# Kernel optimization log

Hardware: AMD Instinct MI355X
Metric: run time of the kernel (lower is better)

Reference implementation:

```python
import jax, jax.numpy as jnp
import numpy as np
from jax import lax

BZ, CAPACITY, SEQ_LEN, IN_VAR, N_EDGES = 64, 134, 288, 16, 96


def setup_inputs() -> dict:
    key = jax.random.key(0)
    ks = jax.random.split(key, 9)
    s_gcn = 1.0 / np.sqrt(SEQ_LEN)
    s_conv = 1.0 / np.sqrt(IN_VAR * 3)
    s_fc = 1.0 / np.sqrt(2 * IN_VAR)
    return {
        "src": jax.random.normal(ks[0], (BZ, CAPACITY, SEQ_LEN, IN_VAR), dtype=jnp.float32),
        "feature_edge_index": jax.random.randint(ks[1], (2, N_EDGES), 0, IN_VAR, dtype=jnp.int32),
        # SAGEConv(seq_len, seq_len): out = lin_l(mean_neighbors) + lin_r(x); lin_l has bias
        "Wl": jax.random.uniform(ks[2], (SEQ_LEN, SEQ_LEN), jnp.float32, -s_gcn, s_gcn),
        "Wr": jax.random.uniform(ks[3], (SEQ_LEN, SEQ_LEN), jnp.float32, -s_gcn, s_gcn),
        "b_gcn": jax.random.uniform(ks[4], (SEQ_LEN,), jnp.float32, -s_gcn, s_gcn),
        "conv1_w": jax.random.uniform(ks[5], (IN_VAR, IN_VAR, 3), jnp.float32, -s_conv, s_conv),
        "conv2_w": jax.random.uniform(ks[6], (IN_VAR, IN_VAR, 5), jnp.float32, -s_conv, s_conv),
        "fc_w": jax.random.uniform(ks[7], (IN_VAR, 2 * IN_VAR), jnp.float32, -s_fc, s_fc),
        "fc_b": jax.random.uniform(ks[8], (IN_VAR,), jnp.float32, -s_fc, s_fc),
    }


def reference(src, feature_edge_index, Wl, Wr, b_gcn, conv1_w, conv2_w, fc_w, fc_b):
    bz, cap, S, F = src.shape  # [bz, capacity, seq_len, in_var]
    B = bz * cap
    # node features for the feature graph: [B, in_var, seq_len]
    x2 = src.transpose(0, 1, 3, 2).reshape(B, F, S)
    e_src, e_dst = feature_edge_index[0], feature_edge_index[1]
    # SAGEConv mean aggregation over shared edge_index, vectorized across B graphs
    gathered = x2[:, e_src, :]                                   # [B, E, S]
    agg = jnp.zeros_like(x2).at[:, e_dst, :].add(gathered)       # [B, F, S]
    deg = jnp.zeros((F,), x2.dtype).at[e_dst].add(1.0)
    mean = agg / jnp.maximum(deg, 1.0)[None, :, None]
    feat = (jnp.einsum('bns,ts->bnt', mean, Wl)
            + jnp.einsum('bns,ts->bnt', x2, Wr) + b_gcn)          # [B, F, S]
    fea_fea = feat.reshape(bz, cap, F, S).transpose(0, 1, 3, 2)   # [bz,cap,S,F]
    # dual temporal Conv1d branches (same padding, no bias) on [B, F, S]
    dn = ('NCH', 'OIH', 'NCH')
    c1 = lax.conv_general_dilated(x2, conv1_w, (1,), [(1, 1)], dimension_numbers=dn)
    c2 = lax.conv_general_dilated(x2, conv2_w, (2,), [(2, 2)][:1] * 1, dimension_numbers=dn) if False else lax.conv_general_dilated(x2, conv2_w, (1,), [(2, 2)], dimension_numbers=dn)
    temporal = (c1 + c2).transpose(0, 2, 1).reshape(bz, cap, S, F)
    com = jnp.concatenate([fea_fea, temporal], axis=-1)           # [bz,cap,S,2F]
    com = jnp.einsum('bcsf,of->bcso', com, fc_w) + fc_b
    # dropout is identity in eval mode
    return src + com
```

## Files before the change

### kernel.cpp

```cpp
#include <hip/hip_runtime.h>
#include <hip/hip_bf16.h>

typedef short short8 __attribute__((ext_vector_type(8)));
typedef float float4v __attribute__((ext_vector_type(4)));
typedef unsigned short ushort4v __attribute__((ext_vector_type(4)));

#define BTOT 8576
#define SEQ 288
#define NF 16
#define NB 4
#define SPN 296
#define XTROWS 294
#define XT_USH (XTROWS * 16)
#define XN_USH (16 * SPN)
#define PBN (XT_USH + XN_USH)
#define WCVW 104

__device__ __forceinline__ unsigned short f2b(float f) {
    union { float f; unsigned u; } v; v.f = f;
    unsigned r = v.u + 0x7FFF + ((v.u >> 16) & 1);
    return (unsigned short)(r >> 16);
}
__device__ __forceinline__ float b2f(unsigned short u) {
    union { unsigned u; float f; } v; v.u = ((unsigned)u) << 16; return v.f;
}

__global__ void wcast_kernel(const float* __restrict__ a, const float* __restrict__ b,
                             unsigned short* __restrict__ o) {
    int i = blockIdx.x * 256 + threadIdx.x;
    o[i]         = f2b(a[i]);
    o[82944 + i] = f2b(b[i]);
}

template<int WPRE>
__device__ __forceinline__ short8 ldw(const unsigned short* __restrict__ wb,
                                      const float* __restrict__ wf, int idx) {
    if (WPRE) {
        return *(const short8*)&wb[idx];
    } else {
        const float* p = &wf[idx];
        float4 w0 = *(const float4*)p, w1 = *(const float4*)(p + 4);
        short8 a;
        a[0] = (short)f2b(w0.x); a[1] = (short)f2b(w0.y);
        a[2] = (short)f2b(w0.z); a[3] = (short)f2b(w0.w);
        a[4] = (short)f2b(w1.x); a[5] = (short)f2b(w1.y);
        a[6] = (short)f2b(w1.z); a[7] = (short)f2b(w1.w);
        return a;
    }
}

#define LDB(KK9, B_) do {                                                      \
    const int s0_ = (KK9) * 32;                                                \
    (B_)[0] = *(const short8*)&xsN0[li * SPN + s0_ + 8 * g];                   \
    (B_)[1] = *(const short8*)&xsN1[li * SPN + s0_ + 8 * g];                   \
    (B_)[2] = *(const short8*)&xsN2[li * SPN + s0_ + 8 * g];                   \
    (B_)[3] = *(const short8*)&xsN3[li * SPN + s0_ + 8 * g];                   \
} while (0)

#define LDA(WT_, WF_, KK9, A_) do {                                            \
    const int s0_ = (KK9) * 32;                                                \
    _Pragma("unroll")                                                          \
    for (int m_ = 0; m_ < 3; ++m_)                                             \
        if (m_ < nt) (A_)[m_] = ldw<WPRE>(WT_, WF_, arow[m_] + s0_ + 8 * g);   \
} while (0)

#define MFK(A_, B_) do {                                                       \
    _Pragma("unroll")                                                          \
    for (int m_ = 0; m_ < 3; ++m_)                                             \
        if (m_ < nt) {                                                         \
            _Pragma("unroll")                                                  \
            for (int n_ = 0; n_ < NB; ++n_)                                    \
                acc[m_][n_] = __builtin_amdgcn_mfma_f32_16x16x32_bf16((A_)[m_], (B_)[n_], acc[m_][n_], 0, 0, 0); \
        }                                                                      \
} while (0)

#define GEMM9(WT_, WF_) do {                                                   \
    short8 aC[3], aN[3];                                                       \
    LDA(WT_, WF_, 0, aC);                                                      \
    LDA(WT_, WF_, 1, aN);                                                      \
    _Pragma("unroll")                                                          \
    for (int kk = 0; kk < 9; ++kk) {                                           \
        short8 bb[NB];                                                         \
        LDB(kk, bb);                                                           \
        if (kk & 1) { MFK(aN, bb); if (kk < 7) LDA(WT_, WF_, kk + 2, aN); }    \
        else        { MFK(aC, bb); if (kk < 7) LDA(WT_, WF_, kk + 2, aC); }    \
    }                                                                          \
} while (0)

template<int WPRE>
__global__ __launch_bounds__(512, 4) void stconv_mfma(
    const float* __restrict__ src,
    const int*   __restrict__ eidx,
    const float* __restrict__ Wlf,
    const float* __restrict__ Wrf,
    const unsigned short* __restrict__ Wbf,
    const float* __restrict__ bgcn,
    const float* __restrict__ cw1g,
    const float* __restrict__ cw2g,
    const float* __restrict__ fcwg,
    const float* __restrict__ fcbg,
    float*       __restrict__ out)
{
    __shared__ unsigned short pool[NB * PBN];
    __shared__ unsigned short wcv[16 * WCVW];
    __shared__ unsigned short fcwB[16 * 40];
    __shared__ unsigned short MB[16 * 40];
    __shared__ float fcb[16];

    const int tid  = threadIdx.x;
    const int wav  = tid >> 6;
    const int lane = tid & 63;
    const int li   = lane & 15;
    const int g    = lane >> 4;
    const int b0   = blockIdx.x * NB;

    int bid[NB];
    #pragma unroll
    for (int n = 0; n < NB; ++n) bid[n] = (b0 + n < BTOT) ? (b0 + n) : (BTOT - 1);

    for (int i = tid; i < 16 * 40; i += 512) MB[i] = 0;
    for (int i = tid; i < 16 * WCVW; i += 512) wcv[i] = 0;
    if (tid < NB * 96) {
        int nb2 = tid / 96, r2 = tid % 96;
        int r = r2 >> 4, f = r2 & 15;
        int row = (r < 2) ? r : 288 + r;
        pool[nb2 * PBN + row * 16 + f] = 0;
    }
    __syncthreads();

    {
        #pragma unroll
        for (int i = 0; i < 3; ++i) {
            int u = i * 512 + tid;
            if (u < NB * 288) {
                int nbu = u / 288, blk = u % 288;
                const float* srcb = src + (size_t)bid[nbu & 3] * (SEQ * NF);
                unsigned short* xsTu = pool + nbu * PBN;
                unsigned short* xsNu = pool + nbu * PBN + XT_USH;
                int s0 = (blk >> 2) * 4, f0 = (blk & 3) * 4;
                ushort4v h[4];
                #pragma unroll
                for (int r = 0; r < 4; ++r) {
                    float4 v = *(const float4*)(srcb + (s0 + r) * 16 + f0);
                    h[r][0] = f2b(v.x); h[r][1] = f2b(v.y);
                    h[r][2] = f2b(v.z); h[r][3] = f2b(v.w);
                    *(ushort4v*)&xsTu[(s0 + r + 2) * 16 + f0] = h[r];
                }
                #pragma unroll
                for (int c = 0; c < 4; ++c) {
                    ushort4v w;
                    w[0] = h[0][c]; w[1] = h[1][c]; w[2] = h[2][c]; w[3] = h[3][c];
                    *(ushort4v*)&xsNu[(f0 + c) * SPN + s0] = w;
                }
            }
        }
    }
    for (int j = tid; j < 1280; j += 512) {
        int fo = j / 80, rem = j % 80, fi = rem / 5, d = rem % 5;
        float t = cw2g[(fo * 16 + fi) * 5 + d];
        if (d >= 1 && d <= 3) t += cw1g[(fo * 16 + fi) * 3 + (d - 1)];
        wcv[fo * WCVW + d * 16 + fi] = f2b(t);
    }
    if (tid < 512) fcwB[(tid >> 5) * 40 + (tid & 31)] = f2b(fcwg[tid]);
    if (tid < 16) fcb[tid] = fcbg[tid];
    if (tid < 256) {
        const int d = tid >> 4, f = tid & 15;
        float cnt = 0.0f;
        for (int e = 0; e < 96; ++e) {
            int es = eidx[e], ed = eidx[96 + e];
            cnt += (ed == d && es == f) ? 1.0f : 0.0f;
        }
        float deg = cnt;
        #pragma unroll
        for (int off = 1; off < 16; off <<= 1) deg += __shfl_xor(deg, off);
        MB[d * 40 + f] = f2b(cnt / fmaxf(deg, 1.0f));
    }
    __syncthreads();

    const int t2 = (wav == 0) ? 16 : ((wav == 5) ? 17 : -1);
    const int nt = (t2 >= 0) ? 3 : 2;
    const int tts[3] = {wav, wav + 8, t2};
    const int arow[3] = {(tts[0] * 16 + li) * 288, (tts[1] * 16 + li) * 288,
                         (t2 >= 0) ? ((t2 * 16 + li) * 288) : 0};

    const unsigned short* WblT = Wbf;
    const unsigned short* WbrT = Wbf + 288 * 288;
    const unsigned short* xsN0 = pool + 0 * PBN + XT_USH;
    const unsigned short* xsN1 = pool + 1 * PBN + XT_USH;
    const unsigned short* xsN2 = pool + 2 * PBN + XT_USH;
    const unsigned short* xsN3 = pool + 3 * PBN + XT_USH;

    float4v acc[3][NB];

    #pragma unroll
    for (int m = 0; m < 3; ++m)
        if (m < nt) {
            #pragma unroll
            for (int r = 0; r < 4; ++r) {
                float bv = bgcn[tts[m] * 16 + 4 * g + r];
                #pragma unroll
                for (int n = 0; n < NB; ++n) acc[m][n][r] = bv;
            }
        }
    GEMM9(WbrT, Wrf);
    __syncthreads();

    {
        short8 bm = *(const short8*)&MB[li * 40 + 8 * g];
        #pragma unroll
        for (int it = 0; it < 9; ++it) {
            int u = wav + 8 * it;
            if (u < NB * 18) {
                int nbu = u / 18, st = u % 18;
                unsigned short* xsTu = pool + nbu * PBN;
                unsigned short* msNu = pool + nbu * PBN + XT_USH;
                int s0 = st * 16;
                short8 a = {0, 0, 0, 0, 0, 0, 0, 0};
                if (g < 2) a = *(const short8*)&xsTu[(s0 + li + 2) * 16 + 8 * g];
                float4v c = {0.f, 0.f, 0.f, 0.f};
                c = __builtin_amdgcn_mfma_f32_16x16x32_bf16(a, bm, c, 0, 0, 0);
                ushort4v p;
                #pragma unroll
                for (int r = 0; r < 4; ++r) p[r] = f2b(c[r]);
                *(ushort4v*)&msNu[li * SPN + s0 + 4 * g] = p;
            }
        }
    }
    __syncthreads();

    GEMM9(WblT, Wlf);

    ushort4v p5o[3][NB];
    #pragma unroll
    for (int m = 0; m < 3; ++m)
        if (m < nt) {
            #pragma unroll
            for (int n = 0; n < NB; ++n) {
                #pragma unroll
                for (int r = 0; r < 4; ++r)
                    p5o[m][n][r] = f2b(acc[m][n][r]);
            }
        }

    ushort4v p6o[9];
    {
        short8 cb0 = *(const short8*)&wcv[li * WCVW + 0  + 8 * g];
        short8 cb1 = *(const short8*)&wcv[li * WCVW + 32 + 8 * g];
        short8 cb2 = *(const short8*)&wcv[li * WCVW + 64 + 8 * g];
        const int fi0   = (g & 1) * 8;
        const int dbase = g >> 1;
        #pragma unroll
        for (int it = 0; it < 9; ++it) {
            int u = wav + 8 * it;
            if (u < NB * 18) {
                int nbu = u / 18, st = u % 18;
                const unsigned short* xsTu = pool + nbu * PBN;
                int s0 = st * 16;
                int rbase = (s0 + li + dbase) * 16 + fi0;
                short8 a0 = *(const short8*)&xsTu[rbase];
                short8 a1 = *(const short8*)&xsTu[rbase + 32];
                short8 a2 = *(const short8*)&xsTu[rbase + 64];
                float4v c = {0.f, 0.f, 0.f, 0.f};
                c = __builtin_amdgcn_mfma_f32_16x16x32_bf16(a0, cb0, c, 0, 0, 0);
                c = __builtin_amdgcn_mfma_f32_16x16x32_bf16(a1, cb1, c, 0, 0, 0);
                c = __builtin_amdgcn_mfma_f32_16x16x32_bf16(a2, cb2, c, 0, 0, 0);
                #pragma unroll
                for (int r = 0; r < 4; ++r) p6o[it][r] = f2b(c[r]);
            }
        }
    }

    ushort4v res16[9];
    #pragma unroll
    for (int it = 0; it < 9; ++it) {
        int u = wav + 8 * it;
        if (u < NB * 18) {
            int nbu = u / 18, st = u % 18;
            const unsigned short* xsTu = pool + nbu * PBN;
            int s0 = st * 16;
            #pragma unroll
            for (int r = 0; r < 4; ++r)
                res16[it][r] = xsTu[(s0 + 4 * g + r + 2) * 16 + li];
        }
    }
    __syncthreads();

    {
        #pragma unroll
        for (int m = 0; m < 3; ++m)
            if (m < nt) {
                #pragma unroll
                for (int n = 0; n < NB; ++n) {
                    unsigned short* catn = pool + n * PBN;
                    #pragma unroll
                    for (int r = 0; r < 4; ++r) {
                        int pos = tts[m] * 16 + 4 * g + r;
                        catn[pos * 32 + li] = p5o[m][n][r];
                    }
                }
            }
        #pragma unroll
        for (int it = 0; it < 9; ++it) {
            int u = wav + 8 * it;
            if (u < NB * 18) {
                int nbu = u / 18, st = u % 18;
                unsigned short* catn = pool + nbu * PBN;
                int s0 = st * 16;
                #pragma unroll
                for (int r = 0; r < 4; ++r)
                    catn[(s0 + 4 * g + r) * 32 + 16 + li] = p6o[it][r];
            }
        }
    }
    __syncthreads();

    {
        short8 fb = *(const short8*)&fcwB[li * 40 + 8 * g];
        #pragma unroll
        for (int it = 0; it < 9; ++it) {
            int u = wav + 8 * it;
            if (u < NB * 18) {
                int nbu = u / 18, st = u % 18;
                const unsigned short* catn = pool + nbu * PBN;
                float* outb = out + (size_t)bid[nbu & 3] * (SEQ * NF);
                int s0 = st * 16;
                float4v c;
                #pragma unroll
                for (int r = 0; r < 4; ++r) c[r] = b2f(res16[it][r]) + fcb[li];
                short8 a = *(const short8*)&catn[(s0 + li) * 32 + 8 * g];
                c = __builtin_amdgcn_mfma_f32_16x16x32_bf16(a, fb, c, 0, 0, 0);
                #pragma unroll
                for (int r = 0; r < 4; ++r) outb[(s0 + 4 * g + r) * 16 + li] = c[r];
            }
        }
    }
}

extern "C" void kernel_launch(void* const* d_in, const int* in_sizes, int n_in,
                              void* d_out, int out_size, void* d_ws, size_t ws_size,
                              hipStream_t stream)
{
    const float* src  = (const float*)d_in[0];
    const int*   eidx = (const int*)  d_in[1];
    const float* Wl   = (const float*)d_in[2];
    const float* Wr   = (const float*)d_in[3];
    const float* bgcn = (const float*)d_in[4];
    const float* cw1  = (const float*)d_in[5];
    const float* cw2  = (const float*)d_in[6];
    const float* fcw  = (const float*)d_in[7];
    const float* fcb  = (const float*)d_in[8];
    float* out = (float*)d_out;

    const int grid = (BTOT + NB - 1) / NB;
    const size_t wbytes = (size_t)2 * 288 * 288 * sizeof(unsigned short);
    if (ws_size >= wbytes) {
        wcast_kernel<<<dim3(324), dim3(256), 0, stream>>>(Wl, Wr, (unsigned short*)d_ws);
        stconv_mfma<1><<<dim3(grid), dim3(512), 0, stream>>>(
            src, eidx, Wl, Wr, (const unsigned short*)d_ws,
            bgcn, cw1, cw2, fcw, fcb, out);
    } else {
        stconv_mfma<0><<<dim3(grid), dim3(512), 0, stream>>>(
            src, eidx, Wl, Wr, nullptr,
            bgcn, cw1, cw2, fcw, fcb, out);
    }
}
```

Before: 167.4 us.

## Process epilogue per batch-node to cut live registers

Restructures the epilogue so that the conv branch, residual load, concat write and final FC GEMM run one node block at a time, instead of holding results for all four blocks in registers across one barrier. The bf16 packing of the GEMM accumulators now happens at store time rather than being staged in a separate array. This shrinks the live register footprint, which could raise occupancy, but it raises the barrier count from two to eight and serializes the four blocks' work.

```diff
diff --git a/kernel.cpp b/kernel.cpp
--- a/kernel.cpp
+++ b/kernel.cpp
@@ -230,107 +230,72 @@
 
     GEMM9(WblT, Wlf);
 
-    ushort4v p5o[3][NB];
-    #pragma unroll
-    for (int m = 0; m < 3; ++m)
-        if (m < nt) {
-            #pragma unroll
-            for (int n = 0; n < NB; ++n) {
-                #pragma unroll
-                for (int r = 0; r < 4; ++r)
-                    p5o[m][n][r] = f2b(acc[m][n][r]);
-            }
-        }
-
-    ushort4v p6o[9];
     {
         short8 cb0 = *(const short8*)&wcv[li * WCVW + 0  + 8 * g];
         short8 cb1 = *(const short8*)&wcv[li * WCVW + 32 + 8 * g];
         short8 cb2 = *(const short8*)&wcv[li * WCVW + 64 + 8 * g];
+        short8 fb  = *(const short8*)&fcwB[li * 40 + 8 * g];
         const int fi0   = (g & 1) * 8;
         const int dbase = g >> 1;
         #pragma unroll
-        for (int it = 0; it < 9; ++it) {
-            int u = wav + 8 * it;
-            if (u < NB * 18) {
-                int nbu = u / 18, st = u % 18;
-                const unsigned short* xsTu = pool + nbu * PBN;
-                int s0 = st * 16;
-                int rbase = (s0 + li + dbase) * 16 + fi0;
-                short8 a0 = *(const short8*)&xsTu[rbase];
-                short8 a1 = *(const short8*)&xsTu[rbase + 32];
-                short8 a2 = *(const short8*)&xsTu[rbase + 64];
-                float4v c = {0.f, 0.f, 0.f, 0.f};
-                c = __builtin_amdgcn_mfma_f32_16x16x32_bf16(a0, cb0, c, 0, 0, 0);
-                c = __builtin_amdgcn_mfma_f32_16x16x32_bf16(a1, cb1, c, 0, 0, 0);
-                c = __builtin_amdgcn_mfma_f32_16x16x32_bf16(a2, cb2, c, 0, 0, 0);
-                #pragma unroll
-                for (int r = 0; r < 4; ++r) p6o[it][r] = f2b(c[r]);
-            }
-        }
-    }
-
-    ushort4v res16[9];
-    #pragma unroll
-    for (int it = 0; it < 9; ++it) {
-        int u = wav + 8 * it;
-        if (u < NB * 18) {
-            int nbu = u / 18, st = u % 18;
-            const unsigned short* xsTu = pool + nbu * PBN;
-            int s0 = st * 16;
-            #pragma unroll
-            for (int r = 0; r < 4; ++r)
-                res16[it][r] = xsTu[(s0 + 4 * g + r + 2) * 16 + li];
-        }
-    }
-    __syncthreads();
-
-    {
-        #pragma unroll
-        for (int m = 0; m < 3; ++m)
-            if (m < nt) {
-                #pragma unroll
-                for (int n = 0; n < NB; ++n) {
-                    unsigned short* catn = pool + n * PBN;
+        for (int n = 0; n < NB; ++n) {
+            unsigned short* pooln = pool + n * PBN;
+            ushort4v p6o[3], rr[3];
+            #pragma unroll
+            for (int it = 0; it < 3; ++it) {
+                int st = wav + 8 * it;
+                if (st < 18) {
+                    int s0 = st * 16;
+                    int rbase = (s0 + li + dbase) * 16 + fi0;
+                    short8 a0 = *(const short8*)&pooln[rbase];
+                    short8 a1 = *(const short8*)&pooln[rbase + 32];
+                    short8 a2 = *(const short8*)&pooln[rbase + 64];
+                    float4v c = {0.f, 0.f, 0.f, 0.f};
+                    c = __builtin_amdgcn_mfma_f32_16x16x32_bf16(a0, cb0, c, 0, 0, 0);
+                    c = __builtin_amdgcn_mfma_f32_16x16x32_bf16(a1, cb1, c, 0, 0, 0);
+                    c = __builtin_amdgcn_mfma_f32_16x16x32_bf16(a2, cb2, c, 0, 0, 0);
+                    #pragma unroll
+                    for (int r = 0; r < 4; ++r) {
+                        p6o[it][r] = f2b(c[r]);
+                        rr[it][r]  = pooln[(s0 + 4 * g + r + 2) * 16 + li];
+                    }
+                }
+            }
+            __syncthreads();
+            #pragma unroll
+            for (int m = 0; m < 3; ++m)
+                if (m < nt) {
                     #pragma unroll
                     for (int r = 0; r < 4; ++r) {
                         int pos = tts[m] * 16 + 4 * g + r;
-                        catn[pos * 32 + li] = p5o[m][n][r];
+                        pooln[pos * 32 + li] = f2b(acc[m][n][r]);
                     }
                 }
-            }
-        #pragma unroll
-        for (int it = 0; it < 9; ++it) {
-            int u = wav + 8 * it;
-            if (u < NB * 18) {
-                int nbu = u / 18, st = u % 18;
-                unsigned short* catn = pool + nbu * PBN;
-                int s0 = st * 16;
-                #pragma unroll
-                for (int r = 0; r < 4; ++r)
-                    catn[(s0 + 4 * g + r) * 32 + 16 + li] = p6o[it][r];
-            }
-        }
-    }
-    __syncthreads();
-
-    {
-        short8 fb = *(const short8*)&fcwB[li * 40 + 8 * g];
-        #pragma unroll
-        for (int it = 0; it < 9; ++it) {
-            int u = wav + 8 * it;
-            if (u < NB * 18) {
-                int nbu = u / 18, st = u % 18;
-                const unsigned short* catn = pool + nbu * PBN;
-                float* outb = out + (size_t)bid[nbu & 3] * (SEQ * NF);
-                int s0 = st * 16;
-                float4v c;
-                #pragma unroll
-                for (int r = 0; r < 4; ++r) c[r] = b2f(res16[it][r]) + fcb[li];
-                short8 a = *(const short8*)&catn[(s0 + li) * 32 + 8 * g];
-                c = __builtin_amdgcn_mfma_f32_16x16x32_bf16(a, fb, c, 0, 0, 0);
-                #pragma unroll
-                for (int r = 0; r < 4; ++r) outb[(s0 + 4 * g + r) * 16 + li] = c[r];
+            #pragma unroll
+            for (int it = 0; it < 3; ++it) {
+                int st = wav + 8 * it;
+                if (st < 18) {
+                    int s0 = st * 16;
+                    #pragma unroll
+                    for (int r = 0; r < 4; ++r)
+                        pooln[(s0 + 4 * g + r) * 32 + 16 + li] = p6o[it][r];
+                }
+            }
+            __syncthreads();
+            float* outb = out + (size_t)bid[n] * (SEQ * NF);
+            #pragma unroll
+            for (int it = 0; it < 3; ++it) {
+                int st = wav + 8 * it;
+                if (st < 18) {
+                    int s0 = st * 16;
+                    float4v c;
+                    #pragma unroll
+                    for (int r = 0; r < 4; ++r) c[r] = b2f(rr[it][r]) + fcb[li];
+                    short8 a = *(const short8*)&pooln[(s0 + li) * 32 + 8 * g];
+                    c = __builtin_amdgcn_mfma_f32_16x16x32_bf16(a, fb, c, 0, 0, 0);
+                    #pragma unroll
+                    for (int r = 0; r < 4; ++r) outb[(s0 + 4 * g + r) * 16 + li] = c[r];
+                }
             }
         }
     }
```

Measured after the change: 143.1 us. -14.5%, faster.
